# Optimization experiments

Hardware: AMD Instinct MI355X
Metric: run time of the kernel (lower is better)

## Reference

```python
import jax, jax.numpy as jnp
import numpy as np

B, H, S, D = 1, 16, 4096, 64
NEG = -1.0e9

def setup_inputs() -> dict:
    key = jax.random.key(0)
    kq, kk, kv, km = jax.random.split(key, 4)
    q = jax.random.normal(kq, (B, H, S, D), dtype=jnp.float32)
    k = jax.random.normal(kk, (B, H, S, D), dtype=jnp.float32)
    v = jax.random.normal(kv, (B, H, S, D), dtype=jnp.float32)
    mask = jax.random.randint(km, (1, 1, S, S), 0, 2, dtype=jnp.int32)
    return {"q": q, "k": k, "v": v, "mask": mask}

def reference(q, k, v, mask):
    # BSM=True: q is NOT divided by temperature (matches torch module default)
    attn = jnp.einsum('bhsd,bhtd->bhst', q, k)           # [B,H,S,S]
    attn = jnp.where(mask == 0, NEG, attn)
    attn = jax.nn.softmax(attn, axis=-1)                 # dropout p=0.0 -> identity
    out = jnp.einsum('bhst,bhtd->bhsd', attn, v)         # [B,H,S,D]
    return (out, attn)
```

## Files before the change

kernel.cpp:

```cpp
#include <hip/hip_runtime.h>
#include <cstdint>
#include <cstddef>

typedef unsigned short u16;
typedef unsigned int u32;
typedef __attribute__((ext_vector_type(8))) _Float16 half8;
typedef __attribute__((ext_vector_type(4))) float floatx4;
typedef __attribute__((ext_vector_type(8))) u16 u16x8;

#define H_ 16
#define S_ 4096
#define D_ 64
#define BM 64
#define BN 64
#define MBW (S_ / 32)

__device__ __forceinline__ u16 f2h(float x) {
  union { _Float16 h; u16 u; } c;
  c.h = (_Float16)x;
  return c.u;
}

__device__ __forceinline__ half8 ld16(const u16* p) {
  return *(const half8*)p;
}

__device__ __forceinline__ void glb_pair(const u16* __restrict__ g, int gstride, int tid,
                                         u16x8& a, u16x8& b) {
  int r = tid >> 2, c0 = (tid & 3) * 16;
  const u16* src = g + (size_t)r * gstride + c0;
  a = *(const u16x8*)src;
  b = *(const u16x8*)(src + 8);
}

__device__ __forceinline__ void stage_regs(u16* lds, int tid, u16x8 a, u16x8 b) {
  int r = tid >> 2, cb = (tid & 3) * 2, sw = r & 7;
  u16* base = lds + r * 64;
  int c0 = (cb ^ sw) << 3;
  *(u16x8*)(base + c0) = a;
  *(u16x8*)(base + (c0 ^ 8)) = b;
}

__device__ __forceinline__ void st_attn8(float* __restrict__ p, half8 v) {
  floatx4 f0 = { (float)v[0], (float)v[1], (float)v[2], (float)v[3] };
  floatx4 f1 = { (float)v[4], (float)v[5], (float)v[6], (float)v[7] };
  __builtin_nontemporal_store(f0, (floatx4*)p);
  __builtin_nontemporal_store(f1, (floatx4*)(p + 4));
}

__global__ void prep_qk(const float* __restrict__ q, const float* __restrict__ kk,
                        u16* __restrict__ qb, u16* __restrict__ kb) {
  const size_t N = (size_t)H_ * S_ * D_;
  size_t idx = ((size_t)blockIdx.x * 256 + threadIdx.x) * 8;
  const float* src;
  u16* dst;
  if (idx < N) { src = q + idx; dst = qb + idx; }
  else         { src = kk + (idx - N); dst = kb + (idx - N); }
  float4 f0 = *(const float4*)src;
  float4 f1 = *(const float4*)(src + 4);
  u16x8 o;
  o[0] = f2h(f0.x); o[1] = f2h(f0.y); o[2] = f2h(f0.z); o[3] = f2h(f0.w);
  o[4] = f2h(f1.x); o[5] = f2h(f1.y); o[6] = f2h(f1.z); o[7] = f2h(f1.w);
  *(u16x8*)dst = o;
}

__global__ void prep_vt(const float* __restrict__ v, u16* __restrict__ vt) {
  __shared__ float tile[64][65];
  int h = blockIdx.y, s0 = blockIdx.x * 64;
  int t = threadIdx.x;
  int r = t >> 2, c0 = (t & 3) * 16;
  const float* src = v + ((size_t)(h * S_ + s0 + r)) * D_ + c0;
  #pragma unroll
  for (int i = 0; i < 16; i += 4) {
    float4 f = *(const float4*)(src + i);
    tile[r][c0 + i + 0] = f.x; tile[r][c0 + i + 1] = f.y;
    tile[r][c0 + i + 2] = f.z; tile[r][c0 + i + 3] = f.w;
  }
  __syncthreads();
  u16* dst = vt + ((size_t)(h * D_ + r)) * S_ + s0 + c0;
  u16x8 o0, o1;
  #pragma unroll
  for (int i = 0; i < 8; i++) o0[i] = f2h(tile[c0 + i][r]);
  #pragma unroll
  for (int i = 0; i < 8; i++) o1[i] = f2h(tile[c0 + 8 + i][r]);
  *(u16x8*)dst = o0;
  *(u16x8*)(dst + 8) = o1;
}

__global__ void prep_mask(const int* __restrict__ mask, u32* __restrict__ mb) {
  size_t widx = (size_t)blockIdx.x * 256 + threadIdx.x;
  const int* src = mask + widx * 32;
  u32 bits = 0;
  #pragma unroll
  for (int i = 0; i < 8; i++) {
    int4 m4 = *(const int4*)(src + i * 4);
    bits |= (m4.x != 0 ? 1u : 0u) << (i * 4 + 0);
    bits |= (m4.y != 0 ? 1u : 0u) << (i * 4 + 1);
    bits |= (m4.z != 0 ? 1u : 0u) << (i * 4 + 2);
    bits |= (m4.w != 0 ? 1u : 0u) << (i * 4 + 3);
  }
  mb[widx] = bits;
}

__global__ __launch_bounds__(256, 4)
void attn_fused(const u16* __restrict__ qb, const u16* __restrict__ kb,
                const u16* __restrict__ vt, const u32* __restrict__ mb,
                float* __restrict__ out, float* __restrict__ attn) {
  __shared__ __align__(16) u16 Ks[BN * D_];
  __shared__ __align__(16) u16 Vts[D_ * BN];
  __shared__ __align__(16) u16 Ps[BM * BN];
  __shared__ float Linv[BM];

  const int h = blockIdx.y;
  const int row0 = blockIdx.x * BM;
  const int tid = threadIdx.x;
  const int wave = tid >> 6;
  const int lane = tid & 63;
  const int lrow = lane & 15;
  const int quad = lane >> 4;
  const int lr0 = wave * 16 + quad * 4;
  const int swb = lrow & 7;
  const int ch0 = (quad ^ swb) << 3;
  const int ch1 = ((quad + 4) ^ swb) << 3;
  const int colc = lrow & 7;
  const int colh = lrow >> 3;

  const u16* qrow = qb + ((size_t)h * S_ + row0 + wave * 16 + lrow) * D_;
  const half8 a0 = ld16(qrow + quad * 8);
  const half8 a1 = ld16(qrow + 32 + quad * 8);

  const u16* kbase = kb + (size_t)h * S_ * D_;
  const u16* vbase = vt + (size_t)h * D_ * S_;

  u16x8 kra, krb;
  glb_pair(kbase, D_, tid, kra, krb);
  float rsum[4] = {0.f, 0.f, 0.f, 0.f};
  for (int j0 = 0; j0 < S_; j0 += BN) {
    __syncthreads();
    stage_regs(Ks, tid, kra, krb);
    int jn = (j0 + BN < S_) ? j0 + BN : 0;
    glb_pair(kbase + (size_t)jn * D_, D_, tid, kra, krb);
    __syncthreads();
    u32 mwx[4], mwy[4];
    #pragma unroll
    for (int r = 0; r < 4; r++) {
      const u32* mp = mb + (size_t)(row0 + lr0 + r) * MBW + (j0 >> 5);
      uint2 w = *(const uint2*)mp;
      mwx[r] = w.x; mwy[r] = w.y;
    }
    #pragma unroll
    for (int c = 0; c < 4; c++) {
      const u16* krow = Ks + (c * 16 + lrow) * 64;
      half8 b0 = ld16(krow + ch0);
      half8 b1 = ld16(krow + ch1);
      floatx4 sc = {0.f, 0.f, 0.f, 0.f};
      sc = __builtin_amdgcn_mfma_f32_16x16x32_f16(a0, b0, sc, 0, 0, 0);
      sc = __builtin_amdgcn_mfma_f32_16x16x32_f16(a1, b1, sc, 0, 0, 0);
      const int sh = (c & 1) * 16 + lrow;
      #pragma unroll
      for (int r = 0; r < 4; r++) {
        u32 w = (c < 2) ? mwx[r] : mwy[r];
        rsum[r] += ((w >> sh) & 1u) ? __expf(sc[r]) : 0.f;
      }
    }
  }
  #pragma unroll
  for (int r = 0; r < 4; r++) {
    float s = rsum[r];
    s += __shfl_xor(s, 1);
    s += __shfl_xor(s, 2);
    s += __shfl_xor(s, 4);
    s += __shfl_xor(s, 8);
    if (lrow == 0) Linv[lr0 + r] = 1.0f / s;
  }
  u16x8 vra, vrb;
  glb_pair(kbase, D_, tid, kra, krb);
  glb_pair(vbase, S_, tid, vra, vrb);
  __syncthreads();
  float linv[4];
  #pragma unroll
  for (int r = 0; r < 4; r++) linv[r] = Linv[lr0 + r];

  floatx4 acc[4];
  #pragma unroll
  for (int c = 0; c < 4; c++) acc[c] = (floatx4){0.f, 0.f, 0.f, 0.f};

  float* attnh = attn + (size_t)h * S_ * S_;

  for (int j0 = 0; j0 < S_; j0 += BN) {
    __syncthreads();
    stage_regs(Ks, tid, kra, krb);
    stage_regs(Vts, tid, vra, vrb);
    int jn = (j0 + BN < S_) ? j0 + BN : 0;
    glb_pair(kbase + (size_t)jn * D_, D_, tid, kra, krb);
    glb_pair(vbase + jn, S_, tid, vra, vrb);
    __syncthreads();
    u32 mwx[4], mwy[4];
    #pragma unroll
    for (int r = 0; r < 4; r++) {
      const u32* mp = mb + (size_t)(row0 + lr0 + r) * MBW + (j0 >> 5);
      uint2 w = *(const uint2*)mp;
      mwx[r] = w.x; mwy[r] = w.y;
    }
    #pragma unroll
    for (int c = 0; c < 4; c++) {
      const u16* krow = Ks + (c * 16 + lrow) * 64;
      half8 b0 = ld16(krow + ch0);
      half8 b1 = ld16(krow + ch1);
      floatx4 sc = {0.f, 0.f, 0.f, 0.f};
      sc = __builtin_amdgcn_mfma_f32_16x16x32_f16(a0, b0, sc, 0, 0, 0);
      sc = __builtin_amdgcn_mfma_f32_16x16x32_f16(a1, b1, sc, 0, 0, 0);
      const int sh = (c & 1) * 16 + lrow;
      #pragma unroll
      for (int r = 0; r < 4; r++) {
        u32 w = (c < 2) ? mwx[r] : mwy[r];
        float p = ((w >> sh) & 1u) ? __expf(sc[r]) * linv[r] : 0.f;
        const int prow = lr0 + r;
        Ps[prow * 64 + (((2 * c + colh) ^ (prow & 7)) << 3) + colc] = f2h(p);
      }
    }
    const u16* prow = Ps + (wave * 16 + lrow) * 64;
    half8 p0 = ld16(prow + ch0);
    half8 p1 = ld16(prow + ch1);
    float* arow = attnh + (size_t)(row0 + wave * 16 + lrow) * S_ + j0 + quad * 8;
    st_attn8(arow, p0);
    st_attn8(arow + 32, p1);
    #pragma unroll
    for (int c = 0; c < 4; c++) {
      const u16* vrow = Vts + (c * 16 + lrow) * 64;
      half8 v0 = ld16(vrow + ch0);
      half8 v1 = ld16(vrow + ch1);
      acc[c] = __builtin_amdgcn_mfma_f32_16x16x32_f16(p0, v0, acc[c], 0, 0, 0);
      acc[c] = __builtin_amdgcn_mfma_f32_16x16x32_f16(p1, v1, acc[c], 0, 0, 0);
    }
  }

  #pragma unroll
  for (int c = 0; c < 4; c++) {
    #pragma unroll
    for (int r = 0; r < 4; r++) {
      out[((size_t)(h * S_ + row0 + lr0 + r)) * D_ + c * 16 + lrow] = acc[c][r];
    }
  }
}

extern "C" void kernel_launch(void* const* d_in, const int* in_sizes, int n_in,
                              void* d_out, int out_size, void* d_ws, size_t ws_size,
                              hipStream_t stream) {
  const float* q = (const float*)d_in[0];
  const float* k = (const float*)d_in[1];
  const float* v = (const float*)d_in[2];
  const int* mask = (const int*)d_in[3];
  float* out = (float*)d_out;
  float* attn = out + (size_t)H_ * S_ * D_;

  const size_t N = (size_t)H_ * S_ * D_;
  u16* qb = (u16*)d_ws;
  u16* kb = qb + N;
  u16* vt = kb + N;
  u32* mb = (u32*)(vt + N);

  prep_qk<<<dim3((unsigned)(2 * N / (256 * 8))), 256, 0, stream>>>(q, k, qb, kb);
  prep_vt<<<dim3(S_ / 64, H_), 256, 0, stream>>>(v, vt);
  prep_mask<<<dim3((unsigned)(((size_t)S_ * S_ / 32) / 256)), 256, 0, stream>>>(mask, mb);
  attn_fused<<<dim3(S_ / BM, H_), 256, 0, stream>>>(qb, kb, vt, mb, out, attn);
}
```

Before: 1.447 ms.

## Pre-swizzle K and V into MFMA fragment order and load directly from global

The prep kernels now write K and V in a layout that matches the per-lane MFMA B-operand fragments. This lets the attention kernel load each lane's half8 operands straight from global memory (L2) instead of staging tiles through LDS. The K and V shared buffers, the Linv LDS round trip and all block-wide barriers in both passes are removed. In exchange, every wave issues its own redundant global loads of the same K/V fragments, with no software prefetch across iterations, so latency is exposed to L2/cache behaviour.

```diff
diff --git a/kernel.cpp b/kernel.cpp
--- a/kernel.cpp
+++ b/kernel.cpp
@@ -14,6 +14,7 @@
 #define BM 64
 #define BN 64
 #define MBW (S_ / 32)
+#define HSTRIDE (S_ * D_)
 
 __device__ __forceinline__ u16 f2h(float x) {
   union { _Float16 h; u16 u; } c;
@@ -23,22 +24,6 @@
 
 __device__ __forceinline__ half8 ld16(const u16* p) {
   return *(const half8*)p;
-}
-
-__device__ __forceinline__ void glb_pair(const u16* __restrict__ g, int gstride, int tid,
-                                         u16x8& a, u16x8& b) {
-  int r = tid >> 2, c0 = (tid & 3) * 16;
-  const u16* src = g + (size_t)r * gstride + c0;
-  a = *(const u16x8*)src;
-  b = *(const u16x8*)(src + 8);
-}
-
-__device__ __forceinline__ void stage_regs(u16* lds, int tid, u16x8 a, u16x8 b) {
-  int r = tid >> 2, cb = (tid & 3) * 2, sw = r & 7;
-  u16* base = lds + r * 64;
-  int c0 = (cb ^ sw) << 3;
-  *(u16x8*)(base + c0) = a;
-  *(u16x8*)(base + (c0 ^ 8)) = b;
 }
 
 __device__ __forceinline__ void st_attn8(float* __restrict__ p, half8 v) {
@@ -48,23 +33,32 @@
   __builtin_nontemporal_store(f1, (floatx4*)(p + 4));
 }
 
-__global__ void prep_qk(const float* __restrict__ q, const float* __restrict__ kk,
-                        u16* __restrict__ qb, u16* __restrict__ kb) {
-  const size_t N = (size_t)H_ * S_ * D_;
+__global__ void prep_q(const float* __restrict__ q, u16* __restrict__ qb) {
   size_t idx = ((size_t)blockIdx.x * 256 + threadIdx.x) * 8;
-  const float* src;
-  u16* dst;
-  if (idx < N) { src = q + idx; dst = qb + idx; }
-  else         { src = kk + (idx - N); dst = kb + (idx - N); }
-  float4 f0 = *(const float4*)src;
-  float4 f1 = *(const float4*)(src + 4);
+  float4 f0 = *(const float4*)(q + idx);
+  float4 f1 = *(const float4*)(q + idx + 4);
   u16x8 o;
   o[0] = f2h(f0.x); o[1] = f2h(f0.y); o[2] = f2h(f0.z); o[3] = f2h(f0.w);
   o[4] = f2h(f1.x); o[5] = f2h(f1.y); o[6] = f2h(f1.z); o[7] = f2h(f1.w);
-  *(u16x8*)dst = o;
-}
-
-__global__ void prep_vt(const float* __restrict__ v, u16* __restrict__ vt) {
+  *(u16x8*)(qb + idx) = o;
+}
+
+__global__ void prep_kf(const float* __restrict__ k, u16* __restrict__ kf) {
+  size_t idx = ((size_t)blockIdx.x * 256 + threadIdx.x) * 8;
+  int h = (int)(idx >> 18);
+  int rem = (int)(idx & (HSTRIDE - 1));
+  int s = rem >> 6, d = rem & 63;
+  float4 f0 = *(const float4*)(k + idx);
+  float4 f1 = *(const float4*)(k + idx + 4);
+  u16x8 o;
+  o[0] = f2h(f0.x); o[1] = f2h(f0.y); o[2] = f2h(f0.z); o[3] = f2h(f0.w);
+  o[4] = f2h(f1.x); o[5] = f2h(f1.y); o[6] = f2h(f1.z); o[7] = f2h(f1.w);
+  size_t off = ((size_t)(h * 256 + (s >> 4))) * 1024
+             + (size_t)(d >> 5) * 512 + (size_t)((d >> 3) & 3) * 128 + (size_t)(s & 15) * 8;
+  *(u16x8*)(kf + off) = o;
+}
+
+__global__ void prep_vf(const float* __restrict__ v, u16* __restrict__ vf) {
   __shared__ float tile[64][65];
   int h = blockIdx.y, s0 = blockIdx.x * 64;
   int t = threadIdx.x;
@@ -77,14 +71,17 @@
     tile[r][c0 + i + 2] = f.z; tile[r][c0 + i + 3] = f.w;
   }
   __syncthreads();
-  u16* dst = vt + ((size_t)(h * D_ + r)) * S_ + s0 + c0;
   u16x8 o0, o1;
   #pragma unroll
   for (int i = 0; i < 8; i++) o0[i] = f2h(tile[c0 + i][r]);
   #pragma unroll
   for (int i = 0; i < 8; i++) o1[i] = f2h(tile[c0 + 8 + i][r]);
-  *(u16x8*)dst = o0;
-  *(u16x8*)(dst + 8) = o1;
+  int c = r >> 4, lrow = r & 15;
+  int half = c0 >> 5, quad = (c0 >> 3) & 3;
+  u16* base = vf + (size_t)h * HSTRIDE + (size_t)blockIdx.x * 4096
+            + (size_t)c * 1024 + (size_t)lrow * 8;
+  *(u16x8*)(base + half * 512 + quad * 128) = o0;
+  *(u16x8*)(base + half * 512 + (quad + 1) * 128) = o1;
 }
 
 __global__ void prep_mask(const int* __restrict__ mask, u32* __restrict__ mb) {
@@ -103,13 +100,10 @@
 }
 
 __global__ __launch_bounds__(256, 4)
-void attn_fused(const u16* __restrict__ qb, const u16* __restrict__ kb,
-                const u16* __restrict__ vt, const u32* __restrict__ mb,
+void attn_fused(const u16* __restrict__ qb, const u16* __restrict__ kf,
+                const u16* __restrict__ vf, const u32* __restrict__ mb,
                 float* __restrict__ out, float* __restrict__ attn) {
-  __shared__ __align__(16) u16 Ks[BN * D_];
-  __shared__ __align__(16) u16 Vts[D_ * BN];
   __shared__ __align__(16) u16 Ps[BM * BN];
-  __shared__ float Linv[BM];
 
   const int h = blockIdx.y;
   const int row0 = blockIdx.x * BM;
@@ -129,18 +123,19 @@
   const half8 a0 = ld16(qrow + quad * 8);
   const half8 a1 = ld16(qrow + 32 + quad * 8);
 
-  const u16* kbase = kb + (size_t)h * S_ * D_;
-  const u16* vbase = vt + (size_t)h * D_ * S_;
-
-  u16x8 kra, krb;
-  glb_pair(kbase, D_, tid, kra, krb);
+  const u16* kfh = kf + (size_t)h * HSTRIDE;
+  const u16* vfh = vf + (size_t)h * HSTRIDE;
+  const int loff = lane * 8;
+
   float rsum[4] = {0.f, 0.f, 0.f, 0.f};
   for (int j0 = 0; j0 < S_; j0 += BN) {
-    __syncthreads();
-    stage_regs(Ks, tid, kra, krb);
-    int jn = (j0 + BN < S_) ? j0 + BN : 0;
-    glb_pair(kbase + (size_t)jn * D_, D_, tid, kra, krb);
-    __syncthreads();
+    const u16* kJ = kfh + (size_t)(j0 >> 4) * 1024;
+    half8 kb0[4], kb1[4];
+    #pragma unroll
+    for (int c = 0; c < 4; c++) {
+      kb0[c] = ld16(kJ + c * 1024 + loff);
+      kb1[c] = ld16(kJ + c * 1024 + 512 + loff);
+    }
     u32 mwx[4], mwy[4];
     #pragma unroll
     for (int r = 0; r < 4; r++) {
@@ -150,12 +145,9 @@
     }
     #pragma unroll
     for (int c = 0; c < 4; c++) {
-      const u16* krow = Ks + (c * 16 + lrow) * 64;
-      half8 b0 = ld16(krow + ch0);
-      half8 b1 = ld16(krow + ch1);
       floatx4 sc = {0.f, 0.f, 0.f, 0.f};
-      sc = __builtin_amdgcn_mfma_f32_16x16x32_f16(a0, b0, sc, 0, 0, 0);
-      sc = __builtin_amdgcn_mfma_f32_16x16x32_f16(a1, b1, sc, 0, 0, 0);
+      sc = __builtin_amdgcn_mfma_f32_16x16x32_f16(a0, kb0[c], sc, 0, 0, 0);
+      sc = __builtin_amdgcn_mfma_f32_16x16x32_f16(a1, kb1[c], sc, 0, 0, 0);
       const int sh = (c & 1) * 16 + lrow;
       #pragma unroll
       for (int r = 0; r < 4; r++) {
@@ -164,6 +156,7 @@
       }
     }
   }
+  float linv[4];
   #pragma unroll
   for (int r = 0; r < 4; r++) {
     float s = rsum[r];
@@ -171,15 +164,8 @@
     s += __shfl_xor(s, 2);
     s += __shfl_xor(s, 4);
     s += __shfl_xor(s, 8);
-    if (lrow == 0) Linv[lr0 + r] = 1.0f / s;
-  }
-  u16x8 vra, vrb;
-  glb_pair(kbase, D_, tid, kra, krb);
-  glb_pair(vbase, S_, tid, vra, vrb);
-  __syncthreads();
-  float linv[4];
-  #pragma unroll
-  for (int r = 0; r < 4; r++) linv[r] = Linv[lr0 + r];
+    linv[r] = 1.0f / s;
+  }
 
   floatx4 acc[4];
   #pragma unroll
@@ -188,13 +174,19 @@
   float* attnh = attn + (size_t)h * S_ * S_;
 
   for (int j0 = 0; j0 < S_; j0 += BN) {
-    __syncthreads();
-    stage_regs(Ks, tid, kra, krb);
-    stage_regs(Vts, tid, vra, vrb);
-    int jn = (j0 + BN < S_) ? j0 + BN : 0;
-    glb_pair(kbase + (size_t)jn * D_, D_, tid, kra, krb);
-    glb_pair(vbase + jn, S_, tid, vra, vrb);
-    __syncthreads();
+    const u16* kJ = kfh + (size_t)(j0 >> 4) * 1024;
+    const u16* vJ = vfh + (size_t)(j0 >> 6) * 4096;
+    half8 kb0[4], kb1[4], vb0[4], vb1[4];
+    #pragma unroll
+    for (int c = 0; c < 4; c++) {
+      kb0[c] = ld16(kJ + c * 1024 + loff);
+      kb1[c] = ld16(kJ + c * 1024 + 512 + loff);
+    }
+    #pragma unroll
+    for (int c = 0; c < 4; c++) {
+      vb0[c] = ld16(vJ + c * 1024 + loff);
+      vb1[c] = ld16(vJ + c * 1024 + 512 + loff);
+    }
     u32 mwx[4], mwy[4];
     #pragma unroll
     for (int r = 0; r < 4; r++) {
@@ -204,12 +196,9 @@
     }
     #pragma unroll
     for (int c = 0; c < 4; c++) {
-      const u16* krow = Ks + (c * 16 + lrow) * 64;
-      half8 b0 = ld16(krow + ch0);
-      half8 b1 = ld16(krow + ch1);
       floatx4 sc = {0.f, 0.f, 0.f, 0.f};
-      sc = __builtin_amdgcn_mfma_f32_16x16x32_f16(a0, b0, sc, 0, 0, 0);
-      sc = __builtin_amdgcn_mfma_f32_16x16x32_f16(a1, b1, sc, 0, 0, 0);
+      sc = __builtin_amdgcn_mfma_f32_16x16x32_f16(a0, kb0[c], sc, 0, 0, 0);
+      sc = __builtin_amdgcn_mfma_f32_16x16x32_f16(a1, kb1[c], sc, 0, 0, 0);
       const int sh = (c & 1) * 16 + lrow;
       #pragma unroll
       for (int r = 0; r < 4; r++) {
@@ -227,11 +216,8 @@
     st_attn8(arow + 32, p1);
     #pragma unroll
     for (int c = 0; c < 4; c++) {
-      const u16* vrow = Vts + (c * 16 + lrow) * 64;
-      half8 v0 = ld16(vrow + ch0);
-      half8 v1 = ld16(vrow + ch1);
-      acc[c] = __builtin_amdgcn_mfma_f32_16x16x32_f16(p0, v0, acc[c], 0, 0, 0);
-      acc[c] = __builtin_amdgcn_mfma_f32_16x16x32_f16(p1, v1, acc[c], 0, 0, 0);
+      acc[c] = __builtin_amdgcn_mfma_f32_16x16x32_f16(p0, vb0[c], acc[c], 0, 0, 0);
+      acc[c] = __builtin_amdgcn_mfma_f32_16x16x32_f16(p1, vb1[c], acc[c], 0, 0, 0);
     }
   }
 
@@ -256,12 +242,13 @@
 
   const size_t N = (size_t)H_ * S_ * D_;
   u16* qb = (u16*)d_ws;
-  u16* kb = qb + N;
-  u16* vt = kb + N;
-  u32* mb = (u32*)(vt + N);
-
-  prep_qk<<<dim3((unsigned)(2 * N / (256 * 8))), 256, 0, stream>>>(q, k, qb, kb);
-  prep_vt<<<dim3(S_ / 64, H_), 256, 0, stream>>>(v, vt);
+  u16* kfb = qb + N;
+  u16* vfb = kfb + N;
+  u32* mb = (u32*)(vfb + N);
+
+  prep_q<<<dim3((unsigned)(N / (256 * 8))), 256, 0, stream>>>(q, qb);
+  prep_kf<<<dim3((unsigned)(N / (256 * 8))), 256, 0, stream>>>(k, kfb);
+  prep_vf<<<dim3(S_ / 64, H_), 256, 0, stream>>>(v, vfb);
   prep_mask<<<dim3((unsigned)(((size_t)S_ * S_ / 32) / 256)), 256, 0, stream>>>(mask, mb);
-  attn_fused<<<dim3(S_ / BM, H_), 256, 0, stream>>>(qb, kb, vt, mb, out, attn);
-}
+  attn_fused<<<dim3(S_ / BM, H_), 256, 0, stream>>>(qb, kfb, vfb, mb, out, attn);
+}
```

Measured after the change: 1.560 ms. 1.08x slower.
